# Performance work log

Hardware: AMD Instinct MI355X
Metric: run time of the kernel (lower is better)

Reference implementation:

```python
import jax, jax.numpy as jnp
import numpy as np

N, K, D = 50000, 16, 128
EPS = 1e-5

def _linear_params(key, fan_in, shape_w, shape_b):
    k1, k2 = jax.random.split(key)
    s = 1.0 / np.sqrt(fan_in)
    W = jax.random.uniform(k1, shape_w, minval=-s, maxval=s, dtype=jnp.float32)
    b = jax.random.uniform(k2, shape_b, minval=-s, maxval=s, dtype=jnp.float32)
    return W, b

def setup_inputs() -> dict:
    key = jax.random.key(0)
    ks = jax.random.split(key, 9)
    Wh, bh = _linear_params(ks[0], D, (D, D), (D,))
    Wt, bt = _linear_params(ks[1], D, (D, D), (D,))
    W1, b1 = _linear_params(ks[2], D, (D, D), (D,))
    W2, b2 = _linear_params(ks[3], D, (D, D), (D,))
    return {
        "x": jax.random.normal(ks[4], (N, D), dtype=jnp.float32),
        "e_h_input": jax.random.normal(ks[5], (N, D), dtype=jnp.float32),
        "e_t_input": jax.random.normal(ks[6], (N, D), dtype=jnp.float32),
        "topk_indices": jax.random.randint(ks[7], (N, K), 0, N),
        "topk_weights": jax.random.uniform(ks[8], (N, K), dtype=jnp.float32),
        "Wh": Wh, "bh": bh, "Wt": Wt, "bt": bt,
        "W1": W1, "b1": b1, "W2": W2, "b2": b2,
        "gamma": jnp.ones((D,), jnp.float32),
        "beta": jnp.zeros((D,), jnp.float32),
    }

def reference(x, e_h_input, e_t_input, topk_indices, topk_weights,
              Wh, bh, Wt, bt, W1, b1, W2, b2, gamma, beta):
    e_h = e_h_input @ Wh.T + bh            # [N, D]
    e_t = e_t_input @ Wt.T + bt            # [N, D]
    Nb_h = e_t[topk_indices]               # [N, K, D] neighbor gather
    p = topk_weights[..., None]            # [N, K, 1]
    e_h_exp = e_h[:, None, :]              # [N, 1, D]
    eh_r = p * Nb_h + (1.0 - p) * e_h_exp  # gated mix
    gate = jnp.tanh(e_h_exp + eh_r)
    ka_prob = jax.nn.softmax(jnp.sum(Nb_h * gate, axis=-1), axis=-1)  # [N, K]
    e_Nh = jnp.einsum('nk,nkd->nd', ka_prob, Nb_h)                    # [N, D]
    sum_emb = jax.nn.leaky_relu((x + e_Nh) @ W1.T + b1, 0.01)
    bi_emb = jax.nn.leaky_relu((x * e_Nh) @ W2.T + b2, 0.01)
    h = sum_emb + bi_emb                   # dropout is identity in eval
    mu = jnp.mean(h, axis=-1, keepdims=True)
    var = jnp.var(h, axis=-1, keepdims=True)
    return (h - mu) / jnp.sqrt(var + EPS) * gamma + beta
```

## Files before the change

kernel.cpp:

```cpp
#include <hip/hip_runtime.h>
#include <stdint.h>

#define NROWS 50000
#define KNB 16
#define DD 128
#define LN_EPS 1e-5f

typedef unsigned short ushort_t;
using frag_ab = __attribute__((ext_vector_type(8))) short;
using frag_cd = __attribute__((ext_vector_type(4))) float;

static __device__ __forceinline__ float bf2f(uint32_t u) {
    union { uint32_t i; float f; } v; v.i = u << 16; return v.f;
}
static __device__ __forceinline__ ushort_t f2bf(float f) {
    union { float f; uint32_t i; } v; v.f = f;
    uint32_t x = v.i;
    return (ushort_t)((x + 0x7fffu + ((x >> 16) & 1u)) >> 16);
}
static __device__ __forceinline__ float leaky(float v) {
    return v > 0.0f ? v : 0.01f * v;
}
static __device__ __forceinline__ float tanh_fast(float z) {
    float e = __expf(2.0f * z);
    return 1.0f - 2.0f / (e + 1.0f);
}
static __device__ __forceinline__ void split_bf(float f, ushort_t& hi, ushort_t& lo) {
    hi = f2bf(f);
    lo = f2bf(f - bf2f(hi));
}
static __device__ __forceinline__ uint32_t cvtpk(float lo, float hi) {
    uint32_t r;
    asm("v_cvt_pk_bf16_f32 %0, %1, %2" : "=v"(r) : "v"(lo), "v"(hi));
    return r;
}
static __device__ __forceinline__ frag_ab load_wfrag(const float* wp) {
    float4 u = *(const float4*)(wp);
    float4 v = *(const float4*)(wp + 4);
    union { uint32_t d[4]; frag_ab f; } r;
    r.d[0] = cvtpk(u.x, u.y);
    r.d[1] = cvtpk(u.z, u.w);
    r.d[2] = cvtpk(v.x, v.y);
    r.d[3] = cvtpk(v.z, v.w);
    return r.f;
}
static __device__ __forceinline__ void load_afrag(const float* ip, frag_ab& hi, frag_ab& lo) {
    float4 u = *(const float4*)(ip);
    float4 v = *(const float4*)(ip + 4);
    float uu[8] = {u.x, u.y, u.z, u.w, v.x, v.y, v.z, v.w};
    #pragma unroll
    for (int i = 0; i < 8; ++i) {
        ushort_t h, l; split_bf(uu[i], h, l);
        hi[i] = (short)h; lo[i] = (short)l;
    }
}

__global__ __launch_bounds__(256, 4) void linear_stream(
    const float* __restrict__ inA, const float* __restrict__ WA,
    const float* __restrict__ bA, float* __restrict__ outA,
    const float* __restrict__ inB, const float* __restrict__ WB,
    const float* __restrict__ bB, float* __restrict__ outB, int half)
{
    const int which = blockIdx.x >= half;
    const int bid   = which ? blockIdx.x - half : blockIdx.x;
    const float* in   = which ? inB : inA;
    const float* W    = which ? WB  : WA;
    const float* bias = which ? bB  : bA;
    float* out        = which ? outB : outA;

    const int tid  = threadIdx.x;
    const int wv   = tid >> 6;
    const int lane = tid & 63;
    const int quad = lane >> 4, lq = lane & 15;
    const int n0   = wv * 32;

    frag_ab BW[2][4];
    #pragma unroll
    for (int t = 0; t < 2; ++t) {
        const float* wr = W + (size_t)(n0 + t * 16 + lq) * DD + quad * 8;
        #pragma unroll
        for (int kc = 0; kc < 4; ++kc)
            BW[t][kc] = load_wfrag(wr + kc * 32);
    }
    float bn[2];
    #pragma unroll
    for (int t = 0; t < 2; ++t) bn[t] = bias[n0 + t * 16 + lq];

    const int ntiles = NROWS / 16;
    for (int t0 = bid; t0 < ntiles; t0 += half) {
        const int r0 = t0 * 16;
        frag_ab Ahi[4], Alo[4];
        const float* ip = in + (size_t)(r0 + lq) * DD + quad * 8;
        #pragma unroll
        for (int kc = 0; kc < 4; ++kc)
            load_afrag(ip + kc * 32, Ahi[kc], Alo[kc]);
        #pragma unroll
        for (int t = 0; t < 2; ++t) {
            frag_cd acc = {0.f, 0.f, 0.f, 0.f};
            #pragma unroll
            for (int kc = 0; kc < 4; ++kc) {
                acc = __builtin_amdgcn_mfma_f32_16x16x32_bf16(Alo[kc], BW[t][kc], acc, 0, 0, 0);
                acc = __builtin_amdgcn_mfma_f32_16x16x32_bf16(Ahi[kc], BW[t][kc], acc, 0, 0, 0);
            }
            #pragma unroll
            for (int r = 0; r < 4; ++r)
                out[(size_t)(r0 + quad * 4 + r) * DD + n0 + t * 16 + lq] = acc[r] + bn[t];
        }
    }
}

__global__ __launch_bounds__(256, 4) void mega_kernel(
    const float* e_h, const float* __restrict__ e_t,
    const int* __restrict__ topk_idx, const float* __restrict__ topk_w,
    const float* __restrict__ x,
    const float* W1, const float* __restrict__ b1,
    const float* W2, const float* __restrict__ b2,
    const float* __restrict__ gamma, const float* __restrict__ beta,
    float* out, int niters)
{
    __shared__ ushort_t aHi[16][136], aLo[16][136];
    __shared__ ushort_t mHi[16][136], mLo[16][136];
    __shared__ float hL[16][132];

    const int tid  = threadIdx.x;
    const int wv   = tid >> 6;
    const int lane = tid & 63;
    const int quad = lane >> 4, lq = lane & 15;
    const int n0   = wv * 32;

    float b1v[2], b2v[2];
    #pragma unroll
    for (int t = 0; t < 2; ++t) {
        b1v[t] = b1[n0 + t * 16 + lq];
        b2v[t] = b2[n0 + t * 16 + lq];
    }
    const float g0 = gamma[lane], g1 = gamma[lane + 64];
    const float be0 = beta[lane], be1 = beta[lane + 64];

    const float* w1p = W1 + (size_t)(n0 + lq) * DD + quad * 8;
    const float* w2p = W2 + (size_t)(n0 + lq) * DD + quad * 8;

    float2 nbb[2][KNB];
    float  pkb[2][KNB];
    float2 ehb[2], xvb[2];

    for (int c = blockIdx.x; c < niters; c += gridDim.x) {
        const int r0 = c << 4;

        {
            const int nu = __builtin_amdgcn_readfirstlane(r0 + 4 * wv);
            #pragma unroll
            for (int k = 0; k < KNB; ++k) {
                int t = topk_idx[nu * KNB + k];
                t = ((unsigned)t < (unsigned)NROWS) ? t : 0;
                nbb[0][k] = *(const float2*)(e_t + (size_t)t * DD + 2 * lane);
            }
            #pragma unroll
            for (int k = 0; k < KNB; ++k) pkb[0][k] = topk_w[nu * KNB + k];
            ehb[0] = *(const float2*)(e_h + (size_t)nu * DD + 2 * lane);
            xvb[0] = *(const float2*)(x   + (size_t)nu * DD + 2 * lane);
        }

        #pragma unroll
        for (int q = 0; q < 4; ++q) {
            const int cur = q & 1, nxt = cur ^ 1;
            if (q < 3) {
                const int nu = __builtin_amdgcn_readfirstlane(r0 + 4 * wv + q + 1);
                #pragma unroll
                for (int k = 0; k < KNB; ++k) {
                    int t = topk_idx[nu * KNB + k];
                    t = ((unsigned)t < (unsigned)NROWS) ? t : 0;
                    nbb[nxt][k] = *(const float2*)(e_t + (size_t)t * DD + 2 * lane);
                }
                #pragma unroll
                for (int k = 0; k < KNB; ++k) pkb[nxt][k] = topk_w[nu * KNB + k];
                ehb[nxt] = *(const float2*)(e_h + (size_t)nu * DD + 2 * lane);
                xvb[nxt] = *(const float2*)(x   + (size_t)nu * DD + 2 * lane);
            }

            const int lr = 4 * wv + q;
            const float2 ehv = ehb[cur];
            const float2 xv  = xvb[cur];
            const float e2x = ehv.x + ehv.x, e2y = ehv.y + ehv.y;

            float s[KNB];
            #pragma unroll
            for (int k = 0; k < KNB; ++k) {
                const float p = pkb[cur][k];
                const float ax = __builtin_fmaf(p, nbb[cur][k].x - ehv.x, e2x);
                const float ay = __builtin_fmaf(p, nbb[cur][k].y - ehv.y, e2y);
                float part = nbb[cur][k].x * tanh_fast(ax)
                           + nbb[cur][k].y * tanh_fast(ay);
                #pragma unroll
                for (int off = 32; off >= 1; off >>= 1)
                    part += __shfl_xor(part, off, 64);
                s[k] = part;
            }
            float mx = s[0];
            #pragma unroll
            for (int k = 1; k < KNB; ++k) mx = fmaxf(mx, s[k]);
            float sum = 0.0f;
            #pragma unroll
            for (int k = 0; k < KNB; ++k) { s[k] = __expf(s[k] - mx); sum += s[k]; }
            const float inv = 1.0f / sum;
            float e0 = 0.0f, e1 = 0.0f;
            #pragma unroll
            for (int k = 0; k < KNB; ++k) { e0 += s[k] * nbb[cur][k].x; e1 += s[k] * nbb[cur][k].y; }
            e0 *= inv; e1 *= inv;

            const float a0 = xv.x + e0, a1 = xv.y + e1;
            const float m0 = xv.x * e0, m1 = xv.y * e1;
            ushort_t h0, l0, h1, l1;
            split_bf(a0, h0, l0); split_bf(a1, h1, l1);
            *(uint32_t*)(&aHi[lr][2 * lane]) = (uint32_t)h0 | ((uint32_t)h1 << 16);
            *(uint32_t*)(&aLo[lr][2 * lane]) = (uint32_t)l0 | ((uint32_t)l1 << 16);
            split_bf(m0, h0, l0); split_bf(m1, h1, l1);
            *(uint32_t*)(&mHi[lr][2 * lane]) = (uint32_t)h0 | ((uint32_t)h1 << 16);
            *(uint32_t*)(&mLo[lr][2 * lane]) = (uint32_t)l0 | ((uint32_t)l1 << 16);
        }
        __syncthreads();

        {
            frag_cd aA0 = {0.f,0.f,0.f,0.f}, aA1 = {0.f,0.f,0.f,0.f};
            frag_cd aM0 = {0.f,0.f,0.f,0.f}, aM1 = {0.f,0.f,0.f,0.f};
            #pragma unroll
            for (int kc = 0; kc < 4; ++kc) {
                frag_ab B10 = load_wfrag(w1p + kc * 32);
                frag_ab B11 = load_wfrag(w1p + 16 * DD + kc * 32);
                frag_ab B20 = load_wfrag(w2p + kc * 32);
                frag_ab B21 = load_wfrag(w2p + 16 * DD + kc * 32);
                frag_ab Ah = *(const frag_ab*)(&aHi[lq][kc * 32 + quad * 8]);
                frag_ab Al = *(const frag_ab*)(&aLo[lq][kc * 32 + quad * 8]);
                frag_ab Mh = *(const frag_ab*)(&mHi[lq][kc * 32 + quad * 8]);
                frag_ab Ml = *(const frag_ab*)(&mLo[lq][kc * 32 + quad * 8]);
                aA0 = __builtin_amdgcn_mfma_f32_16x16x32_bf16(Al, B10, aA0, 0, 0, 0);
                aA0 = __builtin_amdgcn_mfma_f32_16x16x32_bf16(Ah, B10, aA0, 0, 0, 0);
                aA1 = __builtin_amdgcn_mfma_f32_16x16x32_bf16(Al, B11, aA1, 0, 0, 0);
                aA1 = __builtin_amdgcn_mfma_f32_16x16x32_bf16(Ah, B11, aA1, 0, 0, 0);
                aM0 = __builtin_amdgcn_mfma_f32_16x16x32_bf16(Ml, B20, aM0, 0, 0, 0);
                aM0 = __builtin_amdgcn_mfma_f32_16x16x32_bf16(Mh, B20, aM0, 0, 0, 0);
                aM1 = __builtin_amdgcn_mfma_f32_16x16x32_bf16(Ml, B21, aM1, 0, 0, 0);
                aM1 = __builtin_amdgcn_mfma_f32_16x16x32_bf16(Mh, B21, aM1, 0, 0, 0);
            }
            #pragma unroll
            for (int r = 0; r < 4; ++r) {
                const int row = quad * 4 + r;
                hL[row][n0 + lq]      = leaky(aA0[r] + b1v[0]) + leaky(aM0[r] + b2v[0]);
                hL[row][n0 + 16 + lq] = leaky(aA1[r] + b1v[1]) + leaky(aM1[r] + b2v[1]);
            }
        }
        __syncthreads();

        #pragma unroll
        for (int q = 0; q < 4; ++q) {
            const int lr = 4 * wv + q;
            const float h0 = hL[lr][lane], h1 = hL[lr][lane + 64];
            float s = h0 + h1, qq = h0 * h0 + h1 * h1;
            #pragma unroll
            for (int off = 32; off >= 1; off >>= 1) {
                s  += __shfl_xor(s,  off, 64);
                qq += __shfl_xor(qq, off, 64);
            }
            const float mu  = s * (1.0f / DD);
            const float var = qq * (1.0f / DD) - mu * mu;
            const float rs  = rsqrtf(var + LN_EPS);
            out[(size_t)(r0 + lr) * DD + lane]      = (h0 - mu) * rs * g0 + be0;
            out[(size_t)(r0 + lr) * DD + lane + 64] = (h1 - mu) * rs * g1 + be1;
        }
        __syncthreads();
    }
}

extern "C" void kernel_launch(void* const* d_in, const int* in_sizes, int n_in,
                              void* d_out, int out_size, void* d_ws, size_t ws_size,
                              hipStream_t stream) {
    const float* x      = (const float*)d_in[0];
    const float* ehi    = (const float*)d_in[1];
    const float* eti    = (const float*)d_in[2];
    const int*   tidx   = (const int*)d_in[3];
    const float* tw     = (const float*)d_in[4];
    const float* Wh     = (const float*)d_in[5];
    const float* bh     = (const float*)d_in[6];
    const float* Wt     = (const float*)d_in[7];
    const float* bt     = (const float*)d_in[8];
    const float* W1     = (const float*)d_in[9];
    const float* b1     = (const float*)d_in[10];
    const float* W2     = (const float*)d_in[11];
    const float* b2     = (const float*)d_in[12];
    const float* gamma  = (const float*)d_in[13];
    const float* beta   = (const float*)d_in[14];

    float* e_h = (float*)d_out;
    float* e_t = (float*)d_ws;

    const int half = 1024;
    linear_stream<<<2 * half, 256, 0, stream>>>(ehi, Wh, bh, e_h,
                                                eti, Wt, bt, e_t, half);
    mega_kernel<<<1024, 256, 0, stream>>>(e_h, e_t, tidx, tw, x,
                                          W1, b1, W2, b2, gamma, beta,
                                          (float*)d_out, NROWS / 16);
}
```

Before: 310.1 us.

## Process four rows per wave concurrently with 16 lanes per row

Each wave now handles its four rows at once, with 16 lanes per row each owning 8 contiguous features loaded as float4 pairs. This replaces the earlier scheme of one row per wave iteration with register double-buffering. The change shortens the shuffle reduction from 6 steps to 4, vectorizes the index, weight and LDS accesses, and exposes more memory-level parallelism. In exchange it drops the explicit prefetch pipeline and re-gathers the neighbor rows from global memory (likely cache hits) for the weighted sum instead of holding them in registers.

```diff
diff --git a/kernel.cpp b/kernel.cpp
--- a/kernel.cpp
+++ b/kernel.cpp
@@ -118,8 +118,8 @@
     const float* __restrict__ gamma, const float* __restrict__ beta,
     float* out, int niters)
 {
-    __shared__ ushort_t aHi[16][136], aLo[16][136];
-    __shared__ ushort_t mHi[16][136], mLo[16][136];
+    __shared__ __align__(16) ushort_t aHi[16][136], aLo[16][136];
+    __shared__ __align__(16) ushort_t mHi[16][136], mLo[16][136];
     __shared__ float hL[16][132];
 
     const int tid  = threadIdx.x;
@@ -140,61 +140,67 @@
     const float* w1p = W1 + (size_t)(n0 + lq) * DD + quad * 8;
     const float* w2p = W2 + (size_t)(n0 + lq) * DD + quad * 8;
 
-    float2 nbb[2][KNB];
-    float  pkb[2][KNB];
-    float2 ehb[2], xvb[2];
+    const int gA = lane >> 4;
+    const int jA = lane & 15;
 
     for (int c = blockIdx.x; c < niters; c += gridDim.x) {
         const int r0 = c << 4;
 
         {
-            const int nu = __builtin_amdgcn_readfirstlane(r0 + 4 * wv);
+            const int lr = 4 * wv + gA;
+            const int nu = r0 + lr;
+
+            int   adr[KNB];
+            float pk[KNB];
+            {
+                const int*   ipk = topk_idx + (size_t)nu * KNB;
+                const float* wpk = topk_w   + (size_t)nu * KNB;
+                #pragma unroll
+                for (int t = 0; t < 4; ++t) {
+                    int4   t4 = *(const int4*)(ipk + 4 * t);
+                    float4 w4 = *(const float4*)(wpk + 4 * t);
+                    int   tt[4] = {t4.x, t4.y, t4.z, t4.w};
+                    float ww[4] = {w4.x, w4.y, w4.z, w4.w};
+                    #pragma unroll
+                    for (int i = 0; i < 4; ++i) {
+                        int tc = ((unsigned)tt[i] < (unsigned)NROWS) ? tt[i] : 0;
+                        adr[4 * t + i] = tc * DD + 8 * jA;
+                        pk[4 * t + i]  = ww[i];
+                    }
+                }
+            }
+            float eh[8], xv[8];
+            {
+                const float* ehp = e_h + (size_t)nu * DD + 8 * jA;
+                const float* xp  = x   + (size_t)nu * DD + 8 * jA;
+                float4 a0 = *(const float4*)(ehp), a1 = *(const float4*)(ehp + 4);
+                float4 c0 = *(const float4*)(xp),  c1 = *(const float4*)(xp + 4);
+                eh[0]=a0.x; eh[1]=a0.y; eh[2]=a0.z; eh[3]=a0.w;
+                eh[4]=a1.x; eh[5]=a1.y; eh[6]=a1.z; eh[7]=a1.w;
+                xv[0]=c0.x; xv[1]=c0.y; xv[2]=c0.z; xv[3]=c0.w;
+                xv[4]=c1.x; xv[5]=c1.y; xv[6]=c1.z; xv[7]=c1.w;
+            }
+
+            float s[KNB];
             #pragma unroll
             for (int k = 0; k < KNB; ++k) {
-                int t = topk_idx[nu * KNB + k];
-                t = ((unsigned)t < (unsigned)NROWS) ? t : 0;
-                nbb[0][k] = *(const float2*)(e_t + (size_t)t * DD + 2 * lane);
-            }
-            #pragma unroll
-            for (int k = 0; k < KNB; ++k) pkb[0][k] = topk_w[nu * KNB + k];
-            ehb[0] = *(const float2*)(e_h + (size_t)nu * DD + 2 * lane);
-            xvb[0] = *(const float2*)(x   + (size_t)nu * DD + 2 * lane);
-        }
-
-        #pragma unroll
-        for (int q = 0; q < 4; ++q) {
-            const int cur = q & 1, nxt = cur ^ 1;
-            if (q < 3) {
-                const int nu = __builtin_amdgcn_readfirstlane(r0 + 4 * wv + q + 1);
+                const float* nbp = e_t + adr[k];
+                float4 n0v = *(const float4*)(nbp), n1v = *(const float4*)(nbp + 4);
+                float nb[8] = {n0v.x, n0v.y, n0v.z, n0v.w, n1v.x, n1v.y, n1v.z, n1v.w};
+                const float p = pk[k];
+                float acc = 0.0f;
                 #pragma unroll
-                for (int k = 0; k < KNB; ++k) {
-                    int t = topk_idx[nu * KNB + k];
-                    t = ((unsigned)t < (unsigned)NROWS) ? t : 0;
-                    nbb[nxt][k] = *(const float2*)(e_t + (size_t)t * DD + 2 * lane);
+                for (int i = 0; i < 8; ++i) {
+                    const float ax = __builtin_fmaf(p, nb[i] - eh[i], eh[i] + eh[i]);
+                    acc = __builtin_fmaf(nb[i], tanh_fast(ax), acc);
                 }
+                s[k] = acc;
+            }
+            #pragma unroll
+            for (int k = 0; k < KNB; ++k) {
                 #pragma unroll
-                for (int k = 0; k < KNB; ++k) pkb[nxt][k] = topk_w[nu * KNB + k];
-                ehb[nxt] = *(const float2*)(e_h + (size_t)nu * DD + 2 * lane);
-                xvb[nxt] = *(const float2*)(x   + (size_t)nu * DD + 2 * lane);
-            }
-
-            const int lr = 4 * wv + q;
-            const float2 ehv = ehb[cur];
-            const float2 xv  = xvb[cur];
-            const float e2x = ehv.x + ehv.x, e2y = ehv.y + ehv.y;
-
-            float s[KNB];
-            #pragma unroll
-            for (int k = 0; k < KNB; ++k) {
-                const float p = pkb[cur][k];
-                const float ax = __builtin_fmaf(p, nbb[cur][k].x - ehv.x, e2x);
-                const float ay = __builtin_fmaf(p, nbb[cur][k].y - ehv.y, e2y);
-                float part = nbb[cur][k].x * tanh_fast(ax)
-                           + nbb[cur][k].y * tanh_fast(ay);
-                #pragma unroll
-                for (int off = 32; off >= 1; off >>= 1)
-                    part += __shfl_xor(part, off, 64);
-                s[k] = part;
+                for (int off = 8; off >= 1; off >>= 1)
+                    s[k] += __shfl_xor(s[k], off, 64);
             }
             float mx = s[0];
             #pragma unroll
@@ -203,20 +209,40 @@
             #pragma unroll
             for (int k = 0; k < KNB; ++k) { s[k] = __expf(s[k] - mx); sum += s[k]; }
             const float inv = 1.0f / sum;
-            float e0 = 0.0f, e1 = 0.0f;
-            #pragma unroll
-            for (int k = 0; k < KNB; ++k) { e0 += s[k] * nbb[cur][k].x; e1 += s[k] * nbb[cur][k].y; }
-            e0 *= inv; e1 *= inv;
-
-            const float a0 = xv.x + e0, a1 = xv.y + e1;
-            const float m0 = xv.x * e0, m1 = xv.y * e1;
-            ushort_t h0, l0, h1, l1;
-            split_bf(a0, h0, l0); split_bf(a1, h1, l1);
-            *(uint32_t*)(&aHi[lr][2 * lane]) = (uint32_t)h0 | ((uint32_t)h1 << 16);
-            *(uint32_t*)(&aLo[lr][2 * lane]) = (uint32_t)l0 | ((uint32_t)l1 << 16);
-            split_bf(m0, h0, l0); split_bf(m1, h1, l1);
-            *(uint32_t*)(&mHi[lr][2 * lane]) = (uint32_t)h0 | ((uint32_t)h1 << 16);
-            *(uint32_t*)(&mLo[lr][2 * lane]) = (uint32_t)l0 | ((uint32_t)l1 << 16);
+
+            float ea[8] = {0.f,0.f,0.f,0.f,0.f,0.f,0.f,0.f};
+            #pragma unroll
+            for (int k = 0; k < KNB; ++k) {
+                const float w = s[k] * inv;
+                const float* nbp = e_t + adr[k];
+                float4 n0v = *(const float4*)(nbp), n1v = *(const float4*)(nbp + 4);
+                float nb[8] = {n0v.x, n0v.y, n0v.z, n0v.w, n1v.x, n1v.y, n1v.z, n1v.w};
+                #pragma unroll
+                for (int i = 0; i < 8; ++i)
+                    ea[i] = __builtin_fmaf(w, nb[i], ea[i]);
+            }
+
+            uint4 ahv, alv, mhv, mlv;
+            uint32_t* ahp = &ahv.x; uint32_t* alp = &alv.x;
+            uint32_t* mhp = &mhv.x; uint32_t* mlp = &mlv.x;
+            #pragma unroll
+            for (int i = 0; i < 4; ++i) {
+                const float a0 = xv[2*i]   + ea[2*i];
+                const float a1 = xv[2*i+1] + ea[2*i+1];
+                const float m0 = xv[2*i]   * ea[2*i];
+                const float m1 = xv[2*i+1] * ea[2*i+1];
+                ushort_t h0, l0, h1, l1;
+                split_bf(a0, h0, l0); split_bf(a1, h1, l1);
+                ahp[i] = (uint32_t)h0 | ((uint32_t)h1 << 16);
+                alp[i] = (uint32_t)l0 | ((uint32_t)l1 << 16);
+                split_bf(m0, h0, l0); split_bf(m1, h1, l1);
+                mhp[i] = (uint32_t)h0 | ((uint32_t)h1 << 16);
+                mlp[i] = (uint32_t)l0 | ((uint32_t)l1 << 16);
+            }
+            *(uint4*)(&aHi[lr][8 * jA]) = ahv;
+            *(uint4*)(&aLo[lr][8 * jA]) = alv;
+            *(uint4*)(&mHi[lr][8 * jA]) = mhv;
+            *(uint4*)(&mLo[lr][8 * jA]) = mlv;
         }
         __syncthreads();
 
```

Measured after the change: 435.8 us. 40.5% more time.
